# Kernel optimization log

Measured on AMD Instinct MI355X. Metric: run time of the kernel, lower is better.

## Reference

```python
import jax, jax.numpy as jnp
import numpy as np

T = 2048          # tokens (flattened batch*seq, vLLM style)
HID = 2048        # hidden_size
NH = 16           # num_heads
D_NOPE = 128
D_ROPE = 64
D_QK = D_NOPE + D_ROPE   # 192
D_V = 128
Q_LORA = 1536
KV_LORA = 512
THETA = 10000.0
EPS = 1e-6
SCALING = D_QK ** -0.5


def _rmsnorm(x, g):
    return x * jax.lax.rsqrt(jnp.mean(x * x, axis=-1, keepdims=True) + EPS) * g


def _rope(pos, x):
    # interleaved (is_neox_style=False) rotary embedding
    d = x.shape[-1]
    inv = 1.0 / (THETA ** (jnp.arange(0, d, 2, dtype=jnp.float32) / d))
    f = pos.astype(jnp.float32)[:, None] * inv          # [T, d/2]
    cos, sin = jnp.cos(f), jnp.sin(f)
    for _ in range(x.ndim - 2):                          # broadcast over heads
        cos, sin = cos[:, None], sin[:, None]
    x1, x2 = x[..., 0::2], x[..., 1::2]
    o1 = x1 * cos - x2 * sin
    o2 = x1 * sin + x2 * cos
    return jnp.stack([o1, o2], axis=-1).reshape(x.shape)


def setup_inputs() -> dict:
    key = jax.random.key(0)
    ks = jax.random.split(key, 6)
    s = 0.02
    return {
        "hidden_states": jax.random.normal(ks[0], (T, HID), jnp.float32),
        "positions": jnp.arange(T, dtype=jnp.int32),
        "w_qkv_a": jax.random.normal(ks[1], (HID, Q_LORA + KV_LORA + D_ROPE), jnp.float32) * s,
        "g_q": jnp.ones((Q_LORA,), jnp.float32),
        "w_q_b": jax.random.normal(ks[2], (Q_LORA, NH * D_QK), jnp.float32) * s,
        "g_kv": jnp.ones((KV_LORA,), jnp.float32),
        "w_kv_b": jax.random.normal(ks[3], (KV_LORA, NH * (D_NOPE + D_V)), jnp.float32) * s,
        "w_o": jax.random.normal(ks[4], (NH * D_V, HID), jnp.float32) * s,
    }


def reference(hidden_states, positions, w_qkv_a, g_q, w_q_b, g_kv, w_kv_b, w_o):
    # fused low-rank a-projection: [T, q_lora + kv_lora + rope]
    qkv_a = hidden_states @ w_qkv_a
    q_lat = qkv_a[:, :Q_LORA]
    kv_lat = qkv_a[:, Q_LORA:Q_LORA + KV_LORA]
    k_pe = qkv_a[:, Q_LORA + KV_LORA:]                   # [T, rope]

    # query path: rmsnorm -> b-projection -> [T, H, d_qk]
    q = (_rmsnorm(q_lat, g_q) @ w_q_b).reshape(T, NH, D_QK)
    q_nope, q_pe = q[..., :D_NOPE], q[..., D_NOPE:]

    # kv path: rmsnorm -> b-projection -> [T, H, nope + v]
    kv = (_rmsnorm(kv_lat, g_kv) @ w_kv_b).reshape(T, NH, D_NOPE + D_V)
    k_nope, v = kv[..., :D_NOPE], kv[..., D_NOPE:]

    q_pe = _rope(positions, q_pe)                        # [T, H, rope]
    k_pe = _rope(positions, k_pe)                        # [T, rope] shared MQA rope key

    qf = jnp.concatenate([q_nope, q_pe], axis=-1)        # [T, H, d_qk]
    kf = jnp.concatenate([k_nope, jnp.broadcast_to(k_pe[:, None, :], (T, NH, D_ROPE))], axis=-1)

    scores = jnp.einsum("thd,shd->hts", qf, kf) * SCALING   # [H, T, T]
    mask = jnp.tril(jnp.ones((T, T), dtype=bool))
    scores = jnp.where(mask, scores, jnp.finfo(scores.dtype).min)
    probs = jax.nn.softmax(scores, axis=-1)
    out = jnp.einsum("hts,shd->thd", probs, v)           # [T, H, d_v]
    return out.reshape(T, NH * D_V) @ w_o                # [T, hidden]
```

## Files before the change

kernel.cpp:

```cpp
#include <hip/hip_runtime.h>
#include <hip/hip_bf16.h>
#include <math.h>

typedef __bf16 bf16_t;
typedef __bf16 bf16x8 __attribute__((ext_vector_type(8)));
typedef float floatx4 __attribute__((ext_vector_type(4)));
typedef int intx4 __attribute__((ext_vector_type(4)));

#define T_TOK 2048
#define HID 2048
#define NH 16
#define D_NOPE 128
#define D_ROPE 64
#define D_QK 192
#define D_V 128
#define Q_LORA 1536
#define KV_LORA 512
#define QKV_N 2112
#define QKV_NPAD 2176
#define SCALING 0.07216878364870323f
#define LOG2E 1.442695041f
#define EXP_C1 (SCALING * LOG2E)
#define EXP_C2 (12.0f * LOG2E)

#define MFMA_BF16(a, b, c) __builtin_amdgcn_mfma_f32_16x16x32_bf16(a, b, c, 0, 0, 0)

__device__ __forceinline__ void gload16(const void* g, void* l) {
    __builtin_amdgcn_global_load_lds(
        (const __attribute__((address_space(1))) unsigned int*)g,
        (__attribute__((address_space(3))) unsigned int*)l, 16, 0, 0);
}

template <int MODE>
__global__ __launch_bounds__(256) void gemm_mfma(
    const bf16_t* __restrict__ A, const bf16_t* __restrict__ Bt,
    float* __restrict__ Cf, bf16_t* __restrict__ Cb,
    bf16_t* __restrict__ kfull, bf16_t* __restrict__ vtmp,
    int M, int N, int K)
{
    __shared__ __align__(16) bf16_t As[2][2 * 128 * 32];
    __shared__ __align__(16) bf16_t Bs[2][2 * 128 * 32];
    const int tid = threadIdx.x;
    const int lane = tid & 63;
    const int w = tid >> 6;
    const int wm = w >> 1, wn = w & 1;
    const int m0 = blockIdx.y * 128, n0 = blockIdx.x * 128;
    const int l15 = lane & 15, quad = lane >> 4;

    floatx4 acc[4][4] = {};

#define GSTAGE(db_, k0_)                                                                 \
    do {                                                                                 \
        _Pragma("unroll")                                                                \
        for (int it = 0; it < 4; ++it) {                                                 \
            int slot = it * 256 + tid;                                                   \
            int kk2 = slot >> 9;                                                         \
            int r = (slot >> 2) & 127;                                                   \
            int c = slot & 3;                                                            \
            gload16((const char*)(A + (size_t)(m0 + r) * K + (k0_) + kk2 * 32 + c * 8),  \
                    (char*)As[db_] + slot * 16);                                         \
            gload16((const char*)(Bt + (size_t)(n0 + r) * K + (k0_) + kk2 * 32 + c * 8), \
                    (char*)Bs[db_] + slot * 16);                                         \
        }                                                                                \
    } while (0)

    GSTAGE(0, 0);
    int db = 0;
    for (int k0 = 0; k0 < K; k0 += 64) {
        __syncthreads();
        if (k0 + 64 < K) GSTAGE(db ^ 1, k0 + 64);
#pragma unroll
        for (int kk2 = 0; kk2 < 2; ++kk2) {
            bf16x8 af[4], bfr[4];
#pragma unroll
            for (int mi = 0; mi < 4; ++mi)
                af[mi] = *(const bf16x8*)(As[db] + kk2 * 4096 +
                                          (wm * 64 + mi * 16 + l15) * 32 + quad * 8);
#pragma unroll
            for (int ni = 0; ni < 4; ++ni)
                bfr[ni] = *(const bf16x8*)(Bs[db] + kk2 * 4096 +
                                           (wn * 64 + ni * 16 + l15) * 32 + quad * 8);
#pragma unroll
            for (int mi = 0; mi < 4; ++mi)
#pragma unroll
                for (int ni = 0; ni < 4; ++ni)
                    acc[mi][ni] = MFMA_BF16(af[mi], bfr[ni], acc[mi][ni]);
        }
        db ^= 1;
    }
#undef GSTAGE

#pragma unroll
    for (int mi = 0; mi < 4; ++mi)
#pragma unroll
        for (int ni = 0; ni < 4; ++ni)
#pragma unroll
            for (int r = 0; r < 4; ++r) {
                int row = m0 + wm * 64 + mi * 16 + quad * 4 + r;
                int col = n0 + wn * 64 + ni * 16 + l15;
                float v = acc[mi][ni][r];
                if (MODE == 0) {
                    Cf[(size_t)row * N + col] = v;
                } else if (MODE == 1) {
                    Cb[(size_t)row * N + col] = (bf16_t)v;
                } else {
                    int h = col >> 8, dd = col & 255;
                    if (dd < 128)
                        kfull[((size_t)h * T_TOK + row) * 192 + dd] = (bf16_t)v;
                    else
                        vtmp[(size_t)row * 2048 + h * 128 + (dd - 128)] = (bf16_t)v;
                }
            }
}

__global__ void transpose_all(const float* __restrict__ w0, const float* __restrict__ w1,
                              const float* __restrict__ w2, const float* __restrict__ w3,
                              bf16_t* __restrict__ o0, bf16_t* __restrict__ o1,
                              bf16_t* __restrict__ o2, bf16_t* __restrict__ o3) {
    const float* in; bf16_t* out; int K, N;
    switch (blockIdx.z) {
        case 0: in = w0; out = o0; K = 2048; N = 2112; break;
        case 1: in = w1; out = o1; K = 1536; N = 3072; break;
        case 2: in = w2; out = o2; K = 512;  N = 4096; break;
        default: in = w3; out = o3; K = 2048; N = 2048; break;
    }
    int n0 = blockIdx.x * 32, k0 = blockIdx.y * 32;
    if (n0 >= N || k0 >= K) return;
    __shared__ float tile[32][33];
    int tx = threadIdx.x, ty = threadIdx.y;
    for (int i = ty; i < 32; i += 8)
        tile[i][tx] = in[(size_t)(k0 + i) * N + n0 + tx];
    __syncthreads();
    for (int i = ty; i < 32; i += 8)
        out[(size_t)(n0 + i) * K + k0 + tx] = (bf16_t)tile[tx][i];
}

__global__ void transpose_b2b(const bf16_t* __restrict__ in, bf16_t* __restrict__ out,
                              int R, int C) {
    __shared__ bf16_t tile[32][33];
    int c0 = blockIdx.x * 32, r0 = blockIdx.y * 32;
    int tx = threadIdx.x, ty = threadIdx.y;
    for (int i = ty; i < 32; i += 8)
        tile[i][tx] = in[(size_t)(r0 + i) * C + c0 + tx];
    __syncthreads();
    for (int i = ty; i < 32; i += 8)
        out[(size_t)(c0 + i) * R + r0 + tx] = tile[tx][i];
}

__global__ void cvt_f2b(const float* __restrict__ in, bf16_t* __restrict__ out, int n) {
    int i = blockIdx.x * 256 + threadIdx.x;
    if (i < n) out[i] = (bf16_t)in[i];
}

__global__ void mid_fuse(const float* __restrict__ qkv_a, const int* __restrict__ pos,
                         const float* __restrict__ g_q, const float* __restrict__ g_kv,
                         bf16_t* __restrict__ qn, bf16_t* __restrict__ kvn,
                         bf16_t* __restrict__ kfull) {
    int t = blockIdx.x, tid = threadIdx.x;
    const float* x = qkv_a + (size_t)t * QKV_NPAD;
    __shared__ float red[256];
    float ss = 0.f;
    for (int c = tid; c < Q_LORA; c += 256) { float v = x[c]; ss += v * v; }
    red[tid] = ss;
    __syncthreads();
    for (int o = 128; o > 0; o >>= 1) {
        if (tid < o) red[tid] += red[tid + o];
        __syncthreads();
    }
    float rq = rsqrtf(red[0] / (float)Q_LORA + 1e-6f);
    __syncthreads();
    ss = 0.f;
    for (int c = Q_LORA + tid; c < Q_LORA + KV_LORA; c += 256) { float v = x[c]; ss += v * v; }
    red[tid] = ss;
    __syncthreads();
    for (int o = 128; o > 0; o >>= 1) {
        if (tid < o) red[tid] += red[tid + o];
        __syncthreads();
    }
    float rkv = rsqrtf(red[0] / (float)KV_LORA + 1e-6f);

    for (int c = tid; c < Q_LORA; c += 256)
        qn[(size_t)t * Q_LORA + c] = (bf16_t)(x[c] * rq * g_q[c]);
    for (int c = tid; c < KV_LORA; c += 256)
        kvn[(size_t)t * KV_LORA + c] = (bf16_t)(x[Q_LORA + c] * rkv * g_kv[c]);

    if (tid < 32) {
        int i = tid;
        double inv = pow(10000.0, -(double)(2 * i) / 64.0);
        double fd = (double)pos[t] * inv;
        float c = (float)cos(fd), s = (float)sin(fd);
        float x1 = x[Q_LORA + KV_LORA + 2 * i], x2 = x[Q_LORA + KV_LORA + 2 * i + 1];
        bf16_t v0 = (bf16_t)(x1 * c - x2 * s);
        bf16_t v1 = (bf16_t)(x1 * s + x2 * c);
#pragma unroll
        for (int h = 0; h < NH; ++h) {
            kfull[((size_t)h * T_TOK + t) * 192 + 128 + 2 * i] = v0;
            kfull[((size_t)h * T_TOK + t) * 192 + 128 + 2 * i + 1] = v1;
        }
    }
}

__global__ void rope_q_kernel(bf16_t* __restrict__ q, const int* __restrict__ pos) {
    int idx = blockIdx.x * blockDim.x + threadIdx.x;
    if (idx >= T_TOK * NH * 32) return;
    int i = idx & 31;
    int h = (idx >> 5) & (NH - 1);
    int t = idx >> 9;
    double inv = pow(10000.0, -(double)(2 * i) / 64.0);
    double fd = (double)pos[t] * inv;
    float c = (float)cos(fd), s = (float)sin(fd);
    bf16_t* base = q + (size_t)t * (NH * D_QK) + h * D_QK + D_NOPE;
    float x1 = (float)base[2 * i], x2 = (float)base[2 * i + 1];
    base[2 * i] = (bf16_t)(x1 * c - x2 * s);
    base[2 * i + 1] = (bf16_t)(x1 * s + x2 * c);
}

__global__ __launch_bounds__(256, 2) void attn_part(
    const bf16_t* __restrict__ qbuf, const bf16_t* __restrict__ kfull,
    const bf16_t* __restrict__ vT,
    bf16_t* __restrict__ oP0, bf16_t* __restrict__ oP1, float* __restrict__ l_part)
{
    const int id = blockIdx.x;
    const int h = id & 15;
    const int c = (id >> 4) & 3;
    const int qt = 15 - (id >> 6);
    const int q0 = qt * 128;
    const int nTile = 2 * (qt + 1);
    const int tbase = nTile >> 2, trem = nTile & 3;
    const int sz = tbase + (c < trem ? 1 : 0);
    const int sBeg = c * tbase + (c < trem ? c : trem);
    const int sEnd = sBeg + sz;
    const int unit = qt * 16 + h;
    const int tid = threadIdx.x, lane = tid & 63, w = tid >> 6;
    const int l15 = lane & 15, quad = lane >> 4;
    const int ckey = (l15 >> 1) & 3;

    __shared__ __align__(16) bf16_t kn2[2][6 * 64 * 32];
    __shared__ __align__(16) bf16_t vt2[2 * 128 * 32];
    __shared__ __align__(16) bf16_t p_s[128 * 64];

    bf16x8 qf[2][6];
#pragma unroll
    for (int st = 0; st < 2; ++st) {
        const bf16_t* qp = qbuf + (size_t)(q0 + w * 32 + st * 16 + l15) * (NH * D_QK) +
                           h * D_QK;
#pragma unroll
        for (int kk = 0; kk < 6; ++kk)
            qf[st][kk] = *(const bf16x8*)(qp + kk * 32 + quad * 8);
    }

    bf16x8 ones;
#pragma unroll
    for (int j = 0; j < 8; ++j) ones[j] = (bf16_t)1.0f;

    floatx4 o[2][8] = {};
    floatx4 lac[2] = {};
    intx4 vreg[4];

#define STAGE_KN(buf_, s0_)                                                              \
    do {                                                                                 \
        _Pragma("unroll")                                                                \
        for (int it = 0; it < 6; ++it) {                                                 \
            int slot = it * 256 + tid;                                                   \
            int kk = slot >> 8, s = (slot >> 2) & 63, cc = slot & 3;                     \
            int cs = cc ^ ((s >> 1) & 3);                                                \
            gload16((const char*)(kfull + ((size_t)h * T_TOK + (s0_) + s) * 192 +        \
                                  kk * 32 + cs * 8),                                     \
                    (char*)kn2[buf_] + slot * 16);                                       \
        }                                                                                \
    } while (0)

#define VLOAD(s0_)                                                                       \
    do {                                                                                 \
        _Pragma("unroll")                                                                \
        for (int it = 0; it < 4; ++it) {                                                 \
            int slot = it * 256 + tid;                                                   \
            int ks = slot >> 9, d = (slot >> 2) & 127, cc = slot & 3;                    \
            vreg[it] = *(const intx4*)(vT + ((size_t)h * 128 + d) * T_TOK + (s0_) +      \
                                       ks * 32 + cc * 8);                                \
        }                                                                                \
    } while (0)

#define VWRITE()                                                                         \
    do {                                                                                 \
        _Pragma("unroll")                                                                \
        for (int it = 0; it < 4; ++it) {                                                 \
            int slot = it * 256 + tid;                                                   \
            int ks = slot >> 9, d = (slot >> 2) & 127, cc = slot & 3;                    \
            *(intx4*)((char*)vt2 +                                                       \
                      (size_t)((ks * 512 + d * 4 + (cc ^ ((d >> 1) & 3))) * 16)) =       \
                vreg[it];                                                                \
        }                                                                                \
    } while (0)

    if (sz > 0) {
        VLOAD(sBeg * 64);
        STAGE_KN(0, sBeg * 64);
        VWRITE();
    }

    for (int si = sBeg; si < sEnd; ++si) {
        const int s0 = si * 64;
        const int buf = (si - sBeg) & 1;
        __syncthreads();
        if (si + 1 < sEnd) {
            VLOAD(s0 + 64);
            STAGE_KN(buf ^ 1, s0 + 64);
        }

        floatx4 s_acc[2][4] = {};
        __builtin_amdgcn_s_setprio(1);
#pragma unroll
        for (int ni = 0; ni < 4; ++ni) {
#pragma unroll
            for (int kk = 0; kk < 6; ++kk) {
                bf16x8 b = *(const bf16x8*)(kn2[buf] + kk * 2048 +
                                            (ni * 16 + l15) * 32 + (quad ^ ckey) * 8);
                s_acc[0][ni] = MFMA_BF16(qf[0][kk], b, s_acc[0][ni]);
                s_acc[1][ni] = MFMA_BF16(qf[1][kk], b, s_acc[1][ni]);
            }
        }
        __builtin_amdgcn_s_setprio(0);

        const bool diag = (si >= 2 * qt);
#pragma unroll
        for (int st = 0; st < 2; ++st)
#pragma unroll
            for (int ni = 0; ni < 4; ++ni)
#pragma unroll
                for (int r = 0; r < 4; ++r) {
                    int prow = w * 32 + st * 16 + quad * 4 + r;
                    int pcol = ni * 16 + l15;
                    float pv = exp2f(s_acc[st][ni][r] * EXP_C1 - EXP_C2);
                    if (diag && (s0 + pcol) > (q0 + prow)) pv = 0.f;
                    p_s[prow * 64 + ((((pcol >> 3) ^ (prow & 7))) << 3) + (pcol & 7)] =
                        (bf16_t)pv;
                }

        __builtin_amdgcn_s_setprio(1);
#pragma unroll
        for (int ks = 0; ks < 2; ++ks) {
            bf16x8 a0, a1;
            {
                int arow = w * 32 + l15;
                a0 = *(const bf16x8*)(p_s + arow * 64 +
                                      (((ks * 4 + quad) ^ (arow & 7)) << 3));
                arow += 16;
                a1 = *(const bf16x8*)(p_s + arow * 64 +
                                      (((ks * 4 + quad) ^ (arow & 7)) << 3));
            }
            lac[0] = MFMA_BF16(a0, ones, lac[0]);
            lac[1] = MFMA_BF16(a1, ones, lac[1]);
#pragma unroll
            for (int ni = 0; ni < 8; ++ni) {
                bf16x8 b = *(const bf16x8*)(vt2 + ks * 4096 +
                                            (ni * 16 + l15) * 32 + (quad ^ ckey) * 8);
                o[0][ni] = MFMA_BF16(a0, b, o[0][ni]);
                o[1][ni] = MFMA_BF16(a1, b, o[1][ni]);
            }
        }
        __builtin_amdgcn_s_setprio(0);

        __syncthreads();
        if (si + 1 < sEnd) VWRITE();
    }

    bf16_t* op = ((c < 2) ? oP0 : oP1) + (size_t)(unit * 2 + (c & 1)) * 128 * 128;
#pragma unroll
    for (int st = 0; st < 2; ++st) {
#pragma unroll
        for (int ni = 0; ni < 8; ++ni)
#pragma unroll
            for (int r = 0; r < 4; ++r) {
                int lrow = w * 32 + st * 16 + quad * 4 + r;
                op[(size_t)lrow * 128 + ni * 16 + l15] = (bf16_t)o[st][ni][r];
            }
        if (l15 == 0)
#pragma unroll
            for (int r = 0; r < 4; ++r) {
                int lrow = w * 32 + st * 16 + quad * 4 + r;
                l_part[((size_t)unit * 4 + c) * 128 + lrow] = lac[st][r];
            }
    }
#undef STAGE_KN
#undef VLOAD
#undef VWRITE
}

__global__ void attn_combine(const bf16_t* __restrict__ oP0,
                             const bf16_t* __restrict__ oP1,
                             const float* __restrict__ l_part,
                             bf16_t* __restrict__ attn_o)
{
    int idx = blockIdx.x * 256 + threadIdx.x;
    int t = idx >> 8, cg = idx & 255;
    int col = cg * 8;
    int h = col >> 7, d = col & 127;
    int qt = t >> 7, lrow = t & 127;
    size_t unit = (size_t)qt * 16 + h;
    const float* lp = l_part + unit * 4 * 128 + lrow;
    float inv = 1.f / (lp[0] + lp[128] + lp[256] + lp[384]);
    size_t r0 = ((unit * 2 + 0) * 128 + lrow) * 128 + d;
    size_t r1 = ((unit * 2 + 1) * 128 + lrow) * 128 + d;
    bf16x8 a0 = *(const bf16x8*)(oP0 + r0);
    bf16x8 a1 = *(const bf16x8*)(oP0 + r1);
    bf16x8 a2 = *(const bf16x8*)(oP1 + r0);
    bf16x8 a3 = *(const bf16x8*)(oP1 + r1);
    bf16x8 out;
#pragma unroll
    for (int j = 0; j < 8; ++j)
        out[j] = (bf16_t)(((float)a0[j] + (float)a1[j] + (float)a2[j] + (float)a3[j]) * inv);
    *(bf16x8*)(attn_o + (size_t)t * (NH * D_V) + col) = out;
}

extern "C" void kernel_launch(void* const* d_in, const int* in_sizes, int n_in,
                              void* d_out, int out_size, void* d_ws, size_t ws_size,
                              hipStream_t stream) {
    const float* hidden = (const float*)d_in[0];
    const int* positions = (const int*)d_in[1];
    const float* w_qkv_a = (const float*)d_in[2];
    const float* g_q = (const float*)d_in[3];
    const float* w_q_b = (const float*)d_in[4];
    const float* g_kv = (const float*)d_in[5];
    const float* w_kv_b = (const float*)d_in[6];
    const float* w_o = (const float*)d_in[7];
    float* out = (float*)d_out;

    char* p = (char*)d_ws;
    float* qkv_a = (float*)p;
    bf16_t* attn_o = (bf16_t*)p;
    p += (size_t)T_TOK * QKV_NPAD * 4;
    bf16_t* hbf = (bf16_t*)p;
    bf16_t* qn = hbf;
    bf16_t* kvn = hbf + (size_t)T_TOK * Q_LORA;
    p += (size_t)T_TOK * HID * 2;
    bf16_t* qbuf = (bf16_t*)p;  p += (size_t)T_TOK * NH * D_QK * 2;
    bf16_t* vtmp = (bf16_t*)p;  p += (size_t)T_TOK * NH * D_V * 2;
    bf16_t* kfull = (bf16_t*)p; p += (size_t)NH * T_TOK * 192 * 2;
    bf16_t* vT = (bf16_t*)p;    p += (size_t)NH * 128 * T_TOK * 2;
    bf16_t* wt_qkv_a = (bf16_t*)p; p += (size_t)QKV_NPAD * HID * 2;
    bf16_t* wt_q_b = (bf16_t*)p;   p += (size_t)3072 * Q_LORA * 2;
    bf16_t* wt_kv_b = (bf16_t*)p;  p += (size_t)4096 * KV_LORA * 2;
    bf16_t* wt_o = (bf16_t*)p;

    bf16_t* oP0 = wt_qkv_a;
    bf16_t* oP1 = (bf16_t*)((char*)d_ws + (size_t)T_TOK * HID * 2);
    float* l_part = (float*)vtmp;

    dim3 tb(32, 8);

    cvt_f2b<<<(T_TOK * HID) / 256, 256, 0, stream>>>(hidden, hbf, T_TOK * HID);
    transpose_all<<<dim3(128, 64, 4), tb, 0, stream>>>(
        w_qkv_a, w_q_b, w_kv_b, w_o, wt_qkv_a, wt_q_b, wt_kv_b, wt_o);

    gemm_mfma<0><<<dim3(QKV_NPAD / 128, T_TOK / 128), 256, 0, stream>>>(
        hbf, wt_qkv_a, qkv_a, nullptr, nullptr, nullptr, T_TOK, QKV_NPAD, HID);

    mid_fuse<<<T_TOK, 256, 0, stream>>>(qkv_a, positions, g_q, g_kv, qn, kvn, kfull);

    gemm_mfma<1><<<dim3(3072 / 128, T_TOK / 128), 256, 0, stream>>>(
        qn, wt_q_b, nullptr, qbuf, nullptr, nullptr, T_TOK, 3072, Q_LORA);
    rope_q_kernel<<<(T_TOK * NH * 32) / 256, 256, 0, stream>>>(qbuf, positions);

    gemm_mfma<2><<<dim3(4096 / 128, T_TOK / 128), 256, 0, stream>>>(
        kvn, wt_kv_b, nullptr, nullptr, kfull, vtmp, T_TOK, 4096, KV_LORA);
    transpose_b2b<<<dim3(HID / 32, T_TOK / 32), tb, 0, stream>>>(vtmp, vT, T_TOK, HID);

    attn_part<<<1024, 256, 0, stream>>>(qbuf, kfull, vT, oP0, oP1, l_part);
    attn_combine<<<(T_TOK * 256) / 256, 256, 0, stream>>>(oP0, oP1, l_part, attn_o);

    gemm_mfma<0><<<dim3(HID / 128, T_TOK / 128), 256, 0, stream>>>(
        attn_o, wt_o, out, nullptr, nullptr, nullptr, T_TOK, HID, NH * D_V);
}
```

Baseline: 349.6 us.

## Merge q/kv b-projection GEMMs into one launch and split-K the fp32 GEMMs

```diff
diff --git a/kernel.cpp b/kernel.cpp
--- a/kernel.cpp
+++ b/kernel.cpp
@@ -32,19 +32,16 @@
 }
 
 template <int MODE>
-__global__ __launch_bounds__(256) void gemm_mfma(
+__device__ __forceinline__ void gemm_body(
     const bf16_t* __restrict__ A, const bf16_t* __restrict__ Bt,
     float* __restrict__ Cf, bf16_t* __restrict__ Cb,
     bf16_t* __restrict__ kfull, bf16_t* __restrict__ vtmp,
-    int M, int N, int K)
+    int N, int K, int m0, int n0, bf16_t* As, bf16_t* Bs)
 {
-    __shared__ __align__(16) bf16_t As[2][2 * 128 * 32];
-    __shared__ __align__(16) bf16_t Bs[2][2 * 128 * 32];
     const int tid = threadIdx.x;
     const int lane = tid & 63;
     const int w = tid >> 6;
     const int wm = w >> 1, wn = w & 1;
-    const int m0 = blockIdx.y * 128, n0 = blockIdx.x * 128;
     const int l15 = lane & 15, quad = lane >> 4;
 
     floatx4 acc[4][4] = {};
@@ -58,9 +55,9 @@
             int r = (slot >> 2) & 127;                                                   \
             int c = slot & 3;                                                            \
             gload16((const char*)(A + (size_t)(m0 + r) * K + (k0_) + kk2 * 32 + c * 8),  \
-                    (char*)As[db_] + slot * 16);                                         \
+                    (char*)(As + (db_)*8192) + slot * 16);                               \
             gload16((const char*)(Bt + (size_t)(n0 + r) * K + (k0_) + kk2 * 32 + c * 8), \
-                    (char*)Bs[db_] + slot * 16);                                         \
+                    (char*)(Bs + (db_)*8192) + slot * 16);                               \
         }                                                                                \
     } while (0)
 
@@ -74,11 +71,11 @@
             bf16x8 af[4], bfr[4];
 #pragma unroll
             for (int mi = 0; mi < 4; ++mi)
-                af[mi] = *(const bf16x8*)(As[db] + kk2 * 4096 +
+                af[mi] = *(const bf16x8*)(As + db * 8192 + kk2 * 4096 +
                                           (wm * 64 + mi * 16 + l15) * 32 + quad * 8);
 #pragma unroll
             for (int ni = 0; ni < 4; ++ni)
-                bfr[ni] = *(const bf16x8*)(Bs[db] + kk2 * 4096 +
+                bfr[ni] = *(const bf16x8*)(Bs + db * 8192 + kk2 * 4096 +
                                            (wn * 64 + ni * 16 + l15) * 32 + quad * 8);
 #pragma unroll
             for (int mi = 0; mi < 4; ++mi)
@@ -99,18 +96,127 @@
                 int row = m0 + wm * 64 + mi * 16 + quad * 4 + r;
                 int col = n0 + wn * 64 + ni * 16 + l15;
                 float v = acc[mi][ni][r];
-                if (MODE == 0) {
-                    Cf[(size_t)row * N + col] = v;
-                } else if (MODE == 1) {
+                if (MODE == 1) {
                     Cb[(size_t)row * N + col] = (bf16_t)v;
-                } else {
+                } else if (MODE == 2) {
                     int h = col >> 8, dd = col & 255;
                     if (dd < 128)
                         kfull[((size_t)h * T_TOK + row) * 192 + dd] = (bf16_t)v;
                     else
                         vtmp[(size_t)row * 2048 + h * 128 + (dd - 128)] = (bf16_t)v;
+                } else {
+                    Cf[(size_t)row * N + col] = v;
                 }
             }
+}
+
+__global__ __launch_bounds__(256) void gemm_dual(
+    const bf16_t* __restrict__ qn, const bf16_t* __restrict__ wqb,
+    bf16_t* __restrict__ qbuf,
+    const bf16_t* __restrict__ kvn, const bf16_t* __restrict__ wkvb,
+    bf16_t* __restrict__ kfull, bf16_t* __restrict__ vtmp)
+{
+    __shared__ __align__(16) bf16_t As[2 * 8192];
+    __shared__ __align__(16) bf16_t Bs[2 * 8192];
+    int id = blockIdx.x;
+    if (id < 384) {
+        gemm_body<1>(qn, wqb, nullptr, qbuf, nullptr, nullptr,
+                     3072, Q_LORA, (id / 24) * 128, (id % 24) * 128, As, Bs);
+    } else {
+        int i2 = id - 384;
+        gemm_body<2>(kvn, wkvb, nullptr, nullptr, kfull, vtmp,
+                     4096, KV_LORA, (i2 / 32) * 128, (i2 % 32) * 128, As, Bs);
+    }
+}
+
+__global__ __launch_bounds__(512) void gemm_sk(
+    const bf16_t* __restrict__ A, const bf16_t* __restrict__ Bt,
+    float* __restrict__ Cf, int N, int K)
+{
+    __shared__ __align__(16) bf16_t As[2 * 2 * 8192];
+    __shared__ __align__(16) bf16_t Bs[2 * 2 * 8192];
+    const int tid512 = threadIdx.x;
+    const int g = tid512 >> 8;
+    const int tid = tid512 & 255;
+    const int lane = tid & 63;
+    const int w = tid >> 6;
+    const int wm = w >> 1, wn = w & 1;
+    const int m0 = blockIdx.y * 128, n0 = blockIdx.x * 128;
+    const int l15 = lane & 15, quad = lane >> 4;
+    const int Khalf = K >> 1;
+    const bf16_t* Ag = A + g * Khalf;
+    const bf16_t* Bg = Bt + g * Khalf;
+    bf16_t* Asg = As + g * 2 * 8192;
+    bf16_t* Bsg = Bs + g * 2 * 8192;
+
+    floatx4 acc[4][4] = {};
+
+#define GSTAGE(db_, k0_)                                                                 \
+    do {                                                                                 \
+        _Pragma("unroll")                                                                \
+        for (int it = 0; it < 4; ++it) {                                                 \
+            int slot = it * 256 + tid;                                                   \
+            int kk2 = slot >> 9;                                                         \
+            int r = (slot >> 2) & 127;                                                   \
+            int c = slot & 3;                                                            \
+            gload16((const char*)(Ag + (size_t)(m0 + r) * K + (k0_) + kk2 * 32 + c * 8), \
+                    (char*)(Asg + (db_)*8192) + slot * 16);                              \
+            gload16((const char*)(Bg + (size_t)(n0 + r) * K + (k0_) + kk2 * 32 + c * 8), \
+                    (char*)(Bsg + (db_)*8192) + slot * 16);                              \
+        }                                                                                \
+    } while (0)
+
+    GSTAGE(0, 0);
+    int db = 0;
+    for (int k0 = 0; k0 < Khalf; k0 += 64) {
+        __syncthreads();
+        if (k0 + 64 < Khalf) GSTAGE(db ^ 1, k0 + 64);
+#pragma unroll
+        for (int kk2 = 0; kk2 < 2; ++kk2) {
+            bf16x8 af[4], bfr[4];
+#pragma unroll
+            for (int mi = 0; mi < 4; ++mi)
+                af[mi] = *(const bf16x8*)(Asg + db * 8192 + kk2 * 4096 +
+                                          (wm * 64 + mi * 16 + l15) * 32 + quad * 8);
+#pragma unroll
+            for (int ni = 0; ni < 4; ++ni)
+                bfr[ni] = *(const bf16x8*)(Bsg + db * 8192 + kk2 * 4096 +
+                                           (wn * 64 + ni * 16 + l15) * 32 + quad * 8);
+#pragma unroll
+            for (int mi = 0; mi < 4; ++mi)
+#pragma unroll
+                for (int ni = 0; ni < 4; ++ni)
+                    acc[mi][ni] = MFMA_BF16(af[mi], bfr[ni], acc[mi][ni]);
+        }
+        db ^= 1;
+    }
+#undef GSTAGE
+
+    __syncthreads();
+    float* R = (float*)As;
+    if (g == 1) {
+#pragma unroll
+        for (int mi = 0; mi < 4; ++mi)
+#pragma unroll
+            for (int ni = 0; ni < 4; ++ni)
+#pragma unroll
+                for (int r = 0; r < 4; ++r)
+                    R[((mi * 4 + ni) * 4 + r) * 256 + tid] = acc[mi][ni][r];
+    }
+    __syncthreads();
+    if (g == 0) {
+#pragma unroll
+        for (int mi = 0; mi < 4; ++mi)
+#pragma unroll
+            for (int ni = 0; ni < 4; ++ni)
+#pragma unroll
+                for (int r = 0; r < 4; ++r) {
+                    int row = m0 + wm * 64 + mi * 16 + quad * 4 + r;
+                    int col = n0 + wn * 64 + ni * 16 + l15;
+                    Cf[(size_t)row * N + col] =
+                        acc[mi][ni][r] + R[((mi * 4 + ni) * 4 + r) * 256 + tid];
+                }
+    }
 }
 
 __global__ void transpose_all(const float* __restrict__ w0, const float* __restrict__ w1,
@@ -453,22 +559,18 @@
     transpose_all<<<dim3(128, 64, 4), tb, 0, stream>>>(
         w_qkv_a, w_q_b, w_kv_b, w_o, wt_qkv_a, wt_q_b, wt_kv_b, wt_o);
 
-    gemm_mfma<0><<<dim3(QKV_NPAD / 128, T_TOK / 128), 256, 0, stream>>>(
-        hbf, wt_qkv_a, qkv_a, nullptr, nullptr, nullptr, T_TOK, QKV_NPAD, HID);
+    gemm_sk<<<dim3(QKV_NPAD / 128, T_TOK / 128), 512, 0, stream>>>(
+        hbf, wt_qkv_a, qkv_a, QKV_NPAD, HID);
 
     mid_fuse<<<T_TOK, 256, 0, stream>>>(qkv_a, positions, g_q, g_kv, qn, kvn, kfull);
 
-    gemm_mfma<1><<<dim3(3072 / 128, T_TOK / 128), 256, 0, stream>>>(
-        qn, wt_q_b, nullptr, qbuf, nullptr, nullptr, T_TOK, 3072, Q_LORA);
+    gemm_dual<<<896, 256, 0, stream>>>(qn, wt_q_b, qbuf, kvn, wt_kv_b, kfull, vtmp);
     rope_q_kernel<<<(T_TOK * NH * 32) / 256, 256, 0, stream>>>(qbuf, positions);
-
-    gemm_mfma<2><<<dim3(4096 / 128, T_TOK / 128), 256, 0, stream>>>(
-        kvn, wt_kv_b, nullptr, nullptr, kfull, vtmp, T_TOK, 4096, KV_LORA);
     transpose_b2b<<<dim3(HID / 32, T_TOK / 32), tb, 0, stream>>>(vtmp, vT, T_TOK, HID);
 
     attn_part<<<1024, 256, 0, stream>>>(qbuf, kfull, vT, oP0, oP1, l_part);
     attn_combine<<<(T_TOK * 256) / 256, 256, 0, stream>>>(oP0, oP1, l_part, attn_o);
 
-    gemm_mfma<0><<<dim3(HID / 128, T_TOK / 128), 256, 0, stream>>>(
-        attn_o, wt_o, out, nullptr, nullptr, nullptr, T_TOK, HID, NH * D_V);
-}
+    gemm_sk<<<dim3(HID / 128, T_TOK / 128), 512, 0, stream>>>(
+        attn_o, wt_o, out, HID, NH * D_V);
+}
```

Result: slower. 359.6 us (+2.9%).

## Triple-buffer GEMM pipeline, swizzle LDS reads, and merge q/kv b-projections

Applied to the files above, without the earlier changes.

```diff
diff --git a/kernel.cpp b/kernel.cpp
--- a/kernel.cpp
+++ b/kernel.cpp
@@ -32,22 +32,21 @@
 }
 
 template <int MODE>
-__global__ __launch_bounds__(256) void gemm_mfma(
+__device__ __forceinline__ void gemm_body(
     const bf16_t* __restrict__ A, const bf16_t* __restrict__ Bt,
     float* __restrict__ Cf, bf16_t* __restrict__ Cb,
     bf16_t* __restrict__ kfull, bf16_t* __restrict__ vtmp,
-    int M, int N, int K)
+    int N, int K, int m0, int n0, bf16_t* As, bf16_t* Bs)
 {
-    __shared__ __align__(16) bf16_t As[2][2 * 128 * 32];
-    __shared__ __align__(16) bf16_t Bs[2][2 * 128 * 32];
     const int tid = threadIdx.x;
     const int lane = tid & 63;
     const int w = tid >> 6;
     const int wm = w >> 1, wn = w & 1;
-    const int m0 = blockIdx.y * 128, n0 = blockIdx.x * 128;
     const int l15 = lane & 15, quad = lane >> 4;
+    const int ckey = (l15 >> 1) & 3;
 
     floatx4 acc[4][4] = {};
+    const int nst = K >> 6;
 
 #define GSTAGE(db_, k0_)                                                                 \
     do {                                                                                 \
@@ -57,36 +56,51 @@
             int kk2 = slot >> 9;                                                         \
             int r = (slot >> 2) & 127;                                                   \
             int c = slot & 3;                                                            \
-            gload16((const char*)(A + (size_t)(m0 + r) * K + (k0_) + kk2 * 32 + c * 8),  \
-                    (char*)As[db_] + slot * 16);                                         \
-            gload16((const char*)(Bt + (size_t)(n0 + r) * K + (k0_) + kk2 * 32 + c * 8), \
-                    (char*)Bs[db_] + slot * 16);                                         \
+            int cs = c ^ ((r >> 1) & 3);                                                 \
+            gload16((const char*)(A + (size_t)(m0 + r) * K + (k0_) + kk2 * 32 + cs * 8), \
+                    (char*)(As + (size_t)(db_)*8192) + slot * 16);                       \
+            gload16((const char*)(Bt + (size_t)(n0 + r) * K + (k0_) + kk2 * 32 + cs * 8),\
+                    (char*)(Bs + (size_t)(db_)*8192) + slot * 16);                       \
         }                                                                                \
     } while (0)
 
     GSTAGE(0, 0);
+    GSTAGE(1, 64);
+    GSTAGE(2, 128);
     int db = 0;
-    for (int k0 = 0; k0 < K; k0 += 64) {
-        __syncthreads();
-        if (k0 + 64 < K) GSTAGE(db ^ 1, k0 + 64);
+    for (int t = 0; t < nst; ++t) {
+        int pend = nst - 1 - t; if (pend > 2) pend = 2;
+        if (pend == 2)      asm volatile("s_waitcnt vmcnt(16)" ::: "memory");
+        else if (pend == 1) asm volatile("s_waitcnt vmcnt(8)" ::: "memory");
+        else                asm volatile("s_waitcnt vmcnt(0)" ::: "memory");
+        __builtin_amdgcn_s_barrier();
+        __builtin_amdgcn_sched_barrier(0);
+        const bf16_t* Ab = As + (size_t)db * 8192;
+        const bf16_t* Bb = Bs + (size_t)db * 8192;
 #pragma unroll
         for (int kk2 = 0; kk2 < 2; ++kk2) {
             bf16x8 af[4], bfr[4];
 #pragma unroll
             for (int mi = 0; mi < 4; ++mi)
-                af[mi] = *(const bf16x8*)(As[db] + kk2 * 4096 +
-                                          (wm * 64 + mi * 16 + l15) * 32 + quad * 8);
+                af[mi] = *(const bf16x8*)(Ab + kk2 * 4096 +
+                                          (wm * 64 + mi * 16 + l15) * 32 +
+                                          (quad ^ ckey) * 8);
 #pragma unroll
             for (int ni = 0; ni < 4; ++ni)
-                bfr[ni] = *(const bf16x8*)(Bs[db] + kk2 * 4096 +
-                                           (wn * 64 + ni * 16 + l15) * 32 + quad * 8);
+                bfr[ni] = *(const bf16x8*)(Bb + kk2 * 4096 +
+                                           (wn * 64 + ni * 16 + l15) * 32 +
+                                           (quad ^ ckey) * 8);
 #pragma unroll
             for (int mi = 0; mi < 4; ++mi)
 #pragma unroll
                 for (int ni = 0; ni < 4; ++ni)
                     acc[mi][ni] = MFMA_BF16(af[mi], bfr[ni], acc[mi][ni]);
         }
-        db ^= 1;
+        asm volatile("s_waitcnt lgkmcnt(0)" ::: "memory");
+        __builtin_amdgcn_sched_barrier(0);
+        __builtin_amdgcn_s_barrier();
+        if (t + 3 < nst) GSTAGE(db, (t + 3) * 64);
+        db = db + 1; if (db == 3) db = 0;
     }
 #undef GSTAGE
 
@@ -99,18 +113,50 @@
                 int row = m0 + wm * 64 + mi * 16 + quad * 4 + r;
                 int col = n0 + wn * 64 + ni * 16 + l15;
                 float v = acc[mi][ni][r];
-                if (MODE == 0) {
-                    Cf[(size_t)row * N + col] = v;
-                } else if (MODE == 1) {
+                if (MODE == 1) {
                     Cb[(size_t)row * N + col] = (bf16_t)v;
-                } else {
+                } else if (MODE == 2) {
                     int h = col >> 8, dd = col & 255;
                     if (dd < 128)
                         kfull[((size_t)h * T_TOK + row) * 192 + dd] = (bf16_t)v;
                     else
                         vtmp[(size_t)row * 2048 + h * 128 + (dd - 128)] = (bf16_t)v;
+                } else {
+                    Cf[(size_t)row * N + col] = v;
                 }
             }
+}
+
+template <int MODE>
+__global__ __launch_bounds__(256) void gemm_mfma(
+    const bf16_t* __restrict__ A, const bf16_t* __restrict__ Bt,
+    float* __restrict__ Cf, bf16_t* __restrict__ Cb,
+    bf16_t* __restrict__ kfull, bf16_t* __restrict__ vtmp,
+    int M, int N, int K)
+{
+    __shared__ __align__(16) bf16_t As[3 * 8192];
+    __shared__ __align__(16) bf16_t Bs[3 * 8192];
+    gemm_body<MODE>(A, Bt, Cf, Cb, kfull, vtmp, N, K,
+                    blockIdx.y * 128, blockIdx.x * 128, As, Bs);
+}
+
+__global__ __launch_bounds__(256) void gemm_dual(
+    const bf16_t* __restrict__ qn, const bf16_t* __restrict__ wqb,
+    bf16_t* __restrict__ qbuf,
+    const bf16_t* __restrict__ kvn, const bf16_t* __restrict__ wkvb,
+    bf16_t* __restrict__ kfull, bf16_t* __restrict__ vtmp)
+{
+    __shared__ __align__(16) bf16_t As[3 * 8192];
+    __shared__ __align__(16) bf16_t Bs[3 * 8192];
+    int id = blockIdx.x;
+    if (id < 384) {
+        gemm_body<1>(qn, wqb, nullptr, qbuf, nullptr, nullptr,
+                     3072, Q_LORA, (id / 24) * 128, (id % 24) * 128, As, Bs);
+    } else {
+        int i2 = id - 384;
+        gemm_body<2>(kvn, wkvb, nullptr, nullptr, kfull, vtmp,
+                     4096, KV_LORA, (i2 / 32) * 128, (i2 % 32) * 128, As, Bs);
+    }
 }
 
 __global__ void transpose_all(const float* __restrict__ w0, const float* __restrict__ w1,
@@ -458,12 +504,8 @@
 
     mid_fuse<<<T_TOK, 256, 0, stream>>>(qkv_a, positions, g_q, g_kv, qn, kvn, kfull);
 
-    gemm_mfma<1><<<dim3(3072 / 128, T_TOK / 128), 256, 0, stream>>>(
-        qn, wt_q_b, nullptr, qbuf, nullptr, nullptr, T_TOK, 3072, Q_LORA);
+    gemm_dual<<<896, 256, 0, stream>>>(qn, wt_q_b, qbuf, kvn, wt_kv_b, kfull, vtmp);
     rope_q_kernel<<<(T_TOK * NH * 32) / 256, 256, 0, stream>>>(qbuf, positions);
-
-    gemm_mfma<2><<<dim3(4096 / 128, T_TOK / 128), 256, 0, stream>>>(
-        kvn, wt_kv_b, nullptr, nullptr, kfull, vtmp, T_TOK, 4096, KV_LORA);
     transpose_b2b<<<dim3(HID / 32, T_TOK / 32), tb, 0, stream>>>(vtmp, vT, T_TOK, HID);
 
     attn_part<<<1024, 256, 0, stream>>>(qbuf, kfull, vT, oP0, oP1, l_part);
```

Result: slower. 385.3 us (+10.2%).
